# Performance work log

Hardware: AMD Instinct MI355X
Metric: run time of the kernel (lower is better)

## Reference

```python
import jax, jax.numpy as jnp
import numpy as np

# TISA RBF basis (helpers l2_dist / rbf_basis in the repo): f_i(d) = a_i * exp(-|b_i| * (d - c_i)^2)

def setup_inputs() -> dict:
    key = jax.random.key(0)
    k = jax.random.split(key, 8)
    B, L, H, D, S, F = 2, 2048, 8, 64, 2, 5
    qs = jax.random.normal(k[0], (B, L, H, D), dtype=jnp.float32)
    ks = jax.random.normal(k[1], (B, L, H, D), dtype=jnp.float32)
    vs = jax.random.normal(k[2], (B, L, H, D), dtype=jnp.float32)
    qs_s = jax.random.uniform(k[3], (B, L, S), dtype=jnp.float32)
    ks_s = jax.random.uniform(k[4], (B, L, S), dtype=jnp.float32)
    a = jax.random.uniform(k[5], (H * F,), dtype=jnp.float32)
    b = jax.random.uniform(k[6], (H * F,), dtype=jnp.float32)
    c = jax.random.normal(k[7], (H * F,), dtype=jnp.float32) * 0.5
    return {"qs": qs, "ks": ks, "vs": vs, "qs_s": qs_s, "ks_s": ks_s, "a": a, "b": b, "c": c}


def _tisa_attention(qs, ks, vs, qs_s, ks_s, a, b, c):
    B, Q, H, D = qs.shape
    F = a.size // H
    aH, bH, cH = (p.reshape(H, F) for p in (a, b, c))
    # pairwise euclidean distance between query and key locations: [B, Q, K]
    diff = qs_s[:, :, None, :] - ks_s[:, None, :, :]
    d = jnp.sqrt(jnp.sum(diff * diff, axis=-1))
    d_ = d[:, None]  # [B, 1, Q, K] broadcast over heads
    # RBF bias summed over F basis functions (small fixed F -> python sum avoids B,H,F,Q,K blowup)
    bias = sum(
        aH[:, f][None, :, None, None]
        * jnp.exp(-jnp.abs(bH[:, f])[None, :, None, None] * (d_ - cH[:, f][None, :, None, None]) ** 2)
        for f in range(F)
    )  # [B, H, Q, K]
    scale = 1.0 / jnp.sqrt(jnp.asarray(D, dtype=qs.dtype))
    scores = jnp.einsum('bqhd,bkhd->bhqk', qs * scale, ks) + bias
    attn = jax.nn.softmax(scores, axis=-1)
    return jnp.einsum('bhqk,bkhd->bqhd', attn, vs)


def reference(qs, ks, vs, qs_s, ks_s, a, b, c):
    # Matches scan_tisa_biased_attention: online-softmax chunking is mathematically
    # identical to a single stable softmax over the full key axis.
    return _tisa_attention(qs, ks, vs, qs_s, ks_s, a, b, c)
```

## Files before the change

kernel.cpp:

```cpp
#include <hip/hip_runtime.h>
#include <cmath>

typedef _Float16 half8 __attribute__((ext_vector_type(8)));
typedef _Float16 half2v __attribute__((ext_vector_type(2)));
typedef float f32x4 __attribute__((ext_vector_type(4)));
typedef float f32x2 __attribute__((ext_vector_type(2)));

#define B_ 2
#define L_ 2048
#define H_ 8
#define D_ 64
#define S_ 2
#define F_ 5
#define LUTN 512
#define LSCALE 362.03867f
#define LOG2E 1.44269504f
#define QSC (0.125f * LOG2E)

#define QOFF 0
#define KOFF 2097152
#define VOFF 4194304
#define WS_NEED 12582912

#define OFF_K 0
#define OFF_V 16384
#define OFF_P 32768
#define OFF_LUT 53248
#define OFF_KSS 57360
#define ARENA_SZ 59408
#define SLOTF (16 * 68 + 16)

#define GLOBAL_LOAD_LDS16(g, l)                                                  \
  __builtin_amdgcn_global_load_lds((const __attribute__((address_space(1))) void*)(g), \
                                   (__attribute__((address_space(3))) void*)(l), 16, 0, 0)

__global__ __launch_bounds__(256, 4)
void tisa_preproc(const float* __restrict__ qs, const float* __restrict__ ks,
                  const float* __restrict__ vs, _Float16* __restrict__ wsh) {
  __shared__ _Float16 Vl[64 * 72];
  const int t = threadIdx.x;
  const int u = blockIdx.x & 31;
  const int bh = blockIdx.x >> 5;
  const size_t base = ((size_t)(bh >> 3) * L_ + (size_t)u * 64) * (H_ * D_) + (size_t)(bh & 7) * D_;

#pragma unroll
  for (int jj = 0; jj < 2; ++jj) {
    int id = t * 2 + jj;
    int row = id >> 3, c = id & 7;
    const float* src = qs + base + (size_t)row * 512 + c * 8;
    f32x4 x0 = ((const f32x4*)src)[0], x1 = ((const f32x4*)src)[1];
    half8 hh;
#pragma unroll
    for (int k = 0; k < 4; ++k) { hh[k] = (_Float16)(x0[k] * QSC); hh[k + 4] = (_Float16)(x1[k] * QSC); }
    *(half8*)&wsh[QOFF + ((size_t)bh * 32 + u) * 4096 + row * 64 + (c ^ (row & 7)) * 8] = hh;
  }
#pragma unroll
  for (int jj = 0; jj < 2; ++jj) {
    int id = t * 2 + jj;
    int tile = id >> 8, row = (id >> 3) & 31, c = id & 7;
    const float* src = ks + base + (size_t)(tile * 32 + row) * 512 + c * 8;
    f32x4 x0 = ((const f32x4*)src)[0], x1 = ((const f32x4*)src)[1];
    half8 hh;
#pragma unroll
    for (int k = 0; k < 4; ++k) { hh[k] = (_Float16)x0[k]; hh[k + 4] = (_Float16)x1[k]; }
    *(half8*)&wsh[KOFF + ((size_t)bh * 64 + u * 2 + tile) * 2048 + row * 64 + (c ^ (row & 7)) * 8] = hh;
  }
  {
    int key = t >> 2, d0 = (t & 3) * 16;
    const float* src = vs + base + (size_t)key * 512 + d0;
    f32x4 a0 = ((const f32x4*)src)[0], a1 = ((const f32x4*)src)[1];
    f32x4 a2 = ((const f32x4*)src)[2], a3 = ((const f32x4*)src)[3];
    half8 h0, h1;
#pragma unroll
    for (int k = 0; k < 4; ++k) {
      h0[k] = (_Float16)a0[k]; h0[k + 4] = (_Float16)a1[k];
      h1[k] = (_Float16)a2[k]; h1[k + 4] = (_Float16)a3[k];
    }
    *(half8*)&Vl[key * 72 + d0] = h0;
    *(half8*)&Vl[key * 72 + d0 + 8] = h1;
  }
  __syncthreads();
#pragma unroll
  for (int jj = 0; jj < 2; ++jj) {
    int id = t * 2 + jj;
    int tile = id >> 8, s = (id >> 3) & 31, cp = id & 7;
    int d = 2 * s + (cp >> 2), kb = (cp & 3) * 8;
    half8 hh;
#pragma unroll
    for (int j = 0; j < 8; ++j) hh[j] = Vl[(tile * 32 + kb + j) * 72 + d];
    *(half8*)&wsh[VOFF + ((size_t)bh * 64 + u * 2 + tile) * 2048 + s * 64 + (cp ^ (s & 7)) * 8] = hh;
  }
}

__global__ __launch_bounds__(1024, 8)
void tisa_attn_main(const float* __restrict__ qs_s, const float* __restrict__ ks_s,
                    const float* __restrict__ ap, const float* __restrict__ bp,
                    const float* __restrict__ cp, const _Float16* __restrict__ wsh,
                    float* __restrict__ out) {
  __shared__ __align__(16) char arena[ARENA_SZ];
  f32x2* LUT2 = (f32x2*)(arena + OFF_LUT);

  const int t = threadIdx.x;
  const int lane = t & 63;
  const int w = t >> 6;
  const int g = w >> 2;
  const int qw = w & 3;
  const int t2 = t & 255;
  const int quad = lane >> 4;
  const int l16 = lane & 15;

  const int qt = blockIdx.x & 31;
  const int bh = blockIdx.x >> 5;
  const int h = bh & 7;
  const int b = bh >> 3;
  const int q0 = qt * 64;

  if (t <= LUTN) {
    float af[F_], nb[F_], cf[F_];
#pragma unroll
    for (int f = 0; f < F_; ++f) {
      af[f] = ap[h * F_ + f];
      nb[f] = -fabsf(bp[h * F_ + f]);
      cf[f] = cp[h * F_ + f];
    }
    float d0 = (float)t * (1.0f / LSCALE), d1 = (float)(t + 1) * (1.0f / LSCALE);
    float s0 = 0.f, s1 = 0.f;
#pragma unroll
    for (int f = 0; f < F_; ++f) {
      float e0 = d0 - cf[f], e1 = d1 - cf[f];
      s0 += af[f] * __expf(nb[f] * (e0 * e0));
      s1 += af[f] * __expf(nb[f] * (e1 * e1));
    }
    float v0 = (s0 - 8.0f) * LOG2E, v1 = (s1 - 8.0f) * LOG2E;
    LUT2[t] = (f32x2){v0, v1 - v0};
  }

  float qx[4], qy[4];
#pragma unroll
  for (int r = 0; r < 4; ++r) {
    int qrow = q0 + qw * 16 + quad * 4 + r;
    qx[r] = qs_s[((size_t)b * L_ + qrow) * 2 + 0] * LSCALE;
    qy[r] = qs_s[((size_t)b * L_ + qrow) * 2 + 1] * LSCALE;
  }

  const _Float16* Qt = wsh + QOFF + ((size_t)bh * 32 + qt) * 4096;
  const _Float16* Kbh = wsh + KOFF + (size_t)bh * 64 * 2048;
  const _Float16* Vbh = wsh + VOFF + (size_t)bh * 64 * 2048;

  if (w < 8)
    GLOBAL_LOAD_LDS16(Qt + w * 512 + lane * 8, arena + OFF_K + w * 1024);
  __syncthreads();

  half8 qA[2];
#pragma unroll
  for (int kb = 0; kb < 2; ++kb)
    qA[kb] = *(const half8*)(arena + OFF_K + (qw * 16 + l16) * 128 +
                             ((kb * 4 + quad) ^ (l16 & 7)) * 16);

  f32x4 oc[4];
#pragma unroll
  for (int df = 0; df < 4; ++df) oc[df] = (f32x4){0.f, 0.f, 0.f, 0.f};
  float lsum[4] = {0.f, 0.f, 0.f, 0.f};

  const _Float16* ksrc = Kbh + (size_t)(g * 16) * 2048 + t2 * 8;
  const _Float16* vsrc = Vbh + (size_t)(g * 16) * 2048 + t2 * 8;
  char* kdst = arena + OFF_K + g * 4096 + qw * 1024;
  char* vdst = arena + OFF_V + g * 4096 + qw * 1024;
  f32x2* kssG = (f32x2*)(arena + OFF_KSS + g * 512);
  _Float16* Pw = (_Float16*)(arena + OFF_P + w * 1280 + quad * 320 + l16 * 2);

  for (int it = 0; it < 16; ++it) {
    __syncthreads();
    GLOBAL_LOAD_LDS16(ksrc, kdst);
    GLOBAL_LOAD_LDS16(vsrc, vdst);
    ksrc += 2048; vsrc += 2048;
    if (t2 < 32) {
      f32x2 c = *(const f32x2*)(ks_s + ((size_t)b * L_ + (g * 16 + it) * 32 + t2) * 2);
      kssG[t2] = (f32x2){c.x * LSCALE, c.y * LSCALE};
    }
    __syncthreads();

    f32x4 acc[2];
#pragma unroll
    for (int nf = 0; nf < 2; ++nf) {
      f32x4 a = (f32x4){0.f, 0.f, 0.f, 0.f};
#pragma unroll
      for (int kb = 0; kb < 2; ++kb) {
        half8 kf = *(const half8*)(arena + OFF_K + g * 4096 + (nf * 16 + l16) * 128 +
                                   ((kb * 4 + quad) ^ (l16 & 7)) * 16);
        a = __builtin_amdgcn_mfma_f32_16x16x32_f16(qA[kb], kf, a, 0, 0, 0);
      }
      acc[nf] = a;
    }

#pragma unroll
    for (int nf = 0; nf < 2; ++nf) {
      f32x2 kc = kssG[nf * 16 + l16];
#pragma unroll
      for (int r = 0; r < 4; ++r) {
        float dx = qx[r] - kc.x, dy = qy[r] - kc.y;
        float tt = sqrtf(fmaf(dx, dx, dy * dy));
        int ii = (int)tt;
        float fr = tt - (float)ii;
        f32x2 e = LUT2[ii];
        float p = __builtin_amdgcn_exp2f(acc[nf][r] + fmaf(fr, e.y, e.x));
        acc[nf][r] = p;
        lsum[r] += p;
        Pw[r * 40 + nf * 16] = (_Float16)p;
      }
    }

    half8 pa = *(const half8*)(arena + OFF_P + w * 1280 + l16 * 80 + quad * 16);
#pragma unroll
    for (int df = 0; df < 4; ++df) {
      half8 vf = *(const half8*)(arena + OFF_V + g * 4096 + (l16 >> 1) * 128 + df * 1024 +
                                 ((((l16 & 1) * 4 + quad) ^ ((l16 >> 1) & 7)) * 16));
      oc[df] = __builtin_amdgcn_mfma_f32_16x16x32_f16(pa, vf, oc[df], 0, 0, 0);
    }
  }

  float lred[4];
#pragma unroll
  for (int r = 0; r < 4; ++r) {
    float s = lsum[r];
    s += __shfl_xor(s, 1);
    s += __shfl_xor(s, 2);
    s += __shfl_xor(s, 4);
    s += __shfl_xor(s, 8);
    lred[r] = s;
  }
  __syncthreads();
  float* slots = (float*)arena;
  if (g >= 2) {
    float* sl = slots + ((g - 2) * 4 + qw) * SLOTF;
#pragma unroll
    for (int df = 0; df < 4; ++df)
#pragma unroll
      for (int r = 0; r < 4; ++r)
        sl[(quad * 4 + r) * 68 + df * 16 + l16] = oc[df][r];
    if (l16 == 0) {
#pragma unroll
      for (int r = 0; r < 4; ++r) sl[16 * 68 + quad * 4 + r] = lred[r];
    }
  }
  __syncthreads();
  if (g < 2) {
    float* sl = slots + (g * 4 + qw) * SLOTF;
#pragma unroll
    for (int df = 0; df < 4; ++df)
#pragma unroll
      for (int r = 0; r < 4; ++r)
        oc[df][r] += sl[(quad * 4 + r) * 68 + df * 16 + l16];
#pragma unroll
    for (int r = 0; r < 4; ++r) lred[r] += sl[16 * 68 + quad * 4 + r];
  }
  if (g == 1) {
    float* sl = slots + (4 + qw) * SLOTF;
#pragma unroll
    for (int df = 0; df < 4; ++df)
#pragma unroll
      for (int r = 0; r < 4; ++r)
        sl[(quad * 4 + r) * 68 + df * 16 + l16] = oc[df][r];
    if (l16 == 0) {
#pragma unroll
      for (int r = 0; r < 4; ++r) sl[16 * 68 + quad * 4 + r] = lred[r];
    }
  }
  __syncthreads();
  if (g == 0) {
    float* sl = slots + (4 + qw) * SLOTF;
    float inv_l[4];
#pragma unroll
    for (int r = 0; r < 4; ++r)
      inv_l[r] = 1.f / (lred[r] + sl[16 * 68 + quad * 4 + r]);
#pragma unroll
    for (int df = 0; df < 4; ++df)
#pragma unroll
      for (int r = 0; r < 4; ++r) {
        int qrow = q0 + qw * 16 + quad * 4 + r;
        float v = oc[df][r] + sl[(quad * 4 + r) * 68 + df * 16 + l16];
        out[((size_t)(b * L_ + qrow)) * (H_ * D_) + h * D_ + df * 16 + l16] = v * inv_l[r];
      }
  }
}

#define KSTR 72
#define PH 72
__global__ __launch_bounds__(512, 4)
void tisa_attn_fallback(const float* __restrict__ qs, const float* __restrict__ ks,
                        const float* __restrict__ vs, const float* __restrict__ qs_s,
                        const float* __restrict__ ks_s, const float* __restrict__ ap,
                        const float* __restrict__ bp, const float* __restrict__ cp,
                        float* __restrict__ out) {
  __shared__ _Float16 Ks[2][64 * KSTR];
  __shared__ _Float16 VT[2][D_ * KSTR];
  __shared__ _Float16 Pf[8][16 * PH];
  __shared__ float kss2[2][64 * 2];
  __shared__ f32x2 LUT2s[LUTN + 1];
  __shared__ float comb[4][16][64];
  __shared__ float combl[4][16];

  const int t = threadIdx.x;
  const int lane = t & 63;
  const int w = t >> 6;
  const int g = w >> 2;
  const int qw = w & 3;
  const int t2 = t & 255;
  const int quad = lane >> 4;
  const int l16 = lane & 15;
  const int qt = blockIdx.x & 31;
  const int bh = blockIdx.x >> 5;
  const int h = bh & 7;
  const int b = bh >> 3;
  const int q0 = qt * 64;

  float af[F_], nb[F_], cf[F_];
#pragma unroll
  for (int f = 0; f < F_; ++f) {
    af[f] = ap[h * F_ + f];
    nb[f] = -fabsf(bp[h * F_ + f]);
    cf[f] = cp[h * F_ + f];
  }
  for (int i = t; i <= LUTN; i += 512) {
    float d0 = (float)i * (1.0f / LSCALE), d1 = (float)(i + 1) * (1.0f / LSCALE);
    float s0 = 0.f, s1 = 0.f;
#pragma unroll
    for (int f = 0; f < F_; ++f) {
      float e0 = d0 - cf[f], e1 = d1 - cf[f];
      s0 += af[f] * __expf(nb[f] * (e0 * e0));
      s1 += af[f] * __expf(nb[f] * (e1 * e1));
    }
    LUT2s[i] = (f32x2){s0 - 8.0f, s1 - 8.0f};
  }
  float qx[4], qy[4];
#pragma unroll
  for (int r = 0; r < 4; ++r) {
    int qrow = q0 + qw * 16 + quad * 4 + r;
    qx[r] = qs_s[(b * L_ + qrow) * S_ + 0];
    qy[r] = qs_s[(b * L_ + qrow) * S_ + 1];
  }
  if (t < 256) {
    const int row = t >> 2, dc = (t & 3) * 16;
    const float* src = qs + (((size_t)(b * L_ + q0 + row)) * H_ + h) * D_ + dc;
    const f32x4* s4 = (const f32x4*)src;
    f32x4 v0 = s4[0], v1 = s4[1], v2 = s4[2], v3 = s4[3];
    half8 w0, w1;
#pragma unroll
    for (int u = 0; u < 4; ++u) {
      w0[u] = (_Float16)(v0[u] * 0.125f); w0[u + 4] = (_Float16)(v1[u] * 0.125f);
      w1[u] = (_Float16)(v2[u] * 0.125f); w1[u + 4] = (_Float16)(v3[u] * 0.125f);
    }
    *(half8*)&Ks[0][row * KSTR + dc] = w0;
    *(half8*)&Ks[0][row * KSTR + dc + 8] = w1;
  }
  __syncthreads();
  half8 qA[2];
#pragma unroll
  for (int kb = 0; kb < 2; ++kb)
    qA[kb] = *(const half8*)&Ks[0][(qw * 16 + l16) * KSTR + kb * 32 + quad * 8];
  f32x4 oc[4];
#pragma unroll
  for (int df = 0; df < 4; ++df) oc[df] = (f32x4){0.f, 0.f, 0.f, 0.f};
  float l_r[4] = {0.f, 0.f, 0.f, 0.f};

  for (int it = 0; it < 16; ++it) {
    const int k0 = (g * 16 + it) * 64;
    __syncthreads();
    {
      const int row = t2 >> 2, dc = (t2 & 3) * 16;
      const float* src = ks + (((size_t)(b * L_ + k0 + row)) * H_ + h) * D_ + dc;
      const f32x4* s4 = (const f32x4*)src;
      f32x4 v0 = s4[0], v1 = s4[1], v2 = s4[2], v3 = s4[3];
      half8 w0, w1;
#pragma unroll
      for (int u = 0; u < 4; ++u) {
        w0[u] = (_Float16)v0[u]; w0[u + 4] = (_Float16)v1[u];
        w1[u] = (_Float16)v2[u]; w1[u + 4] = (_Float16)v3[u];
      }
      *(half8*)&Ks[g][row * KSTR + dc] = w0;
      *(half8*)&Ks[g][row * KSTR + dc + 8] = w1;
    }
    {
      const int kk = (t2 & 31) * 2, dg = (t2 >> 5) * 8;
      const float* s0 = vs + (((size_t)(b * L_ + k0 + kk)) * H_ + h) * D_ + dg;
      const float* s1 = s0 + H_ * D_;
      f32x4 a0 = ((const f32x4*)s0)[0], a1 = ((const f32x4*)s0)[1];
      f32x4 b0 = ((const f32x4*)s1)[0], b1 = ((const f32x4*)s1)[1];
#pragma unroll
      for (int u = 0; u < 4; ++u) {
        half2v p0 = {(_Float16)a0[u], (_Float16)b0[u]};
        *(half2v*)&VT[g][(dg + u) * KSTR + kk] = p0;
        half2v p1 = {(_Float16)a1[u], (_Float16)b1[u]};
        *(half2v*)&VT[g][(dg + 4 + u) * KSTR + kk] = p1;
      }
    }
    if (t2 < 128) kss2[g][t2] = ks_s[((size_t)(b * L_) + k0 + (t2 >> 1)) * S_ + (t2 & 1)];
    __syncthreads();
    f32x4 acc[4];
#pragma unroll
    for (int nf = 0; nf < 4; ++nf) {
      f32x4 a = (f32x4){0.f, 0.f, 0.f, 0.f};
#pragma unroll
      for (int kb = 0; kb < 2; ++kb) {
        half8 kf = *(const half8*)&Ks[g][(nf * 16 + l16) * KSTR + kb * 32 + quad * 8];
        a = __builtin_amdgcn_mfma_f32_16x16x32_f16(qA[kb], kf, a, 0, 0, 0);
      }
      acc[nf] = a;
    }
#pragma unroll
    for (int nf = 0; nf < 4; ++nf) {
      float kx = kss2[g][(nf * 16 + l16) * 2 + 0];
      float ky = kss2[g][(nf * 16 + l16) * 2 + 1];
#pragma unroll
      for (int r = 0; r < 4; ++r) {
        float dx = qx[r] - kx, dy = qy[r] - ky;
        float dist = sqrtf(fmaf(dx, dx, dy * dy));
        float tt = dist * LSCALE;
        int ii = (int)tt;
        float fr = tt - (float)ii;
        f32x2 lh = LUT2s[ii];
        float p = __expf(acc[nf][r] + fmaf(fr, lh.y - lh.x, lh.x));
        acc[nf][r] = p;
      }
    }
#pragma unroll
    for (int r = 0; r < 4; ++r)
      l_r[r] += (acc[0][r] + acc[1][r]) + (acc[2][r] + acc[3][r]);
#pragma unroll
    for (int nf = 0; nf < 4; ++nf)
#pragma unroll
      for (int r = 0; r < 4; ++r)
        Pf[w][(quad * 4 + r) * PH + nf * 16 + l16] = (_Float16)acc[nf][r];
#pragma unroll
    for (int kb = 0; kb < 2; ++kb) {
      half8 pa = *(const half8*)&Pf[w][l16 * PH + kb * 32 + quad * 8];
#pragma unroll
      for (int df = 0; df < 4; ++df) {
        half8 vf = *(const half8*)&VT[g][(df * 16 + l16) * KSTR + kb * 32 + quad * 8];
        oc[df] = __builtin_amdgcn_mfma_f32_16x16x32_f16(pa, vf, oc[df], 0, 0, 0);
      }
    }
  }
  __syncthreads();
  float lred[4];
#pragma unroll
  for (int r = 0; r < 4; ++r) {
    float s = l_r[r];
    s += __shfl_xor(s, 1); s += __shfl_xor(s, 2);
    s += __shfl_xor(s, 4); s += __shfl_xor(s, 8);
    lred[r] = s;
  }
  if (g == 1) {
#pragma unroll
    for (int df = 0; df < 4; ++df)
#pragma unroll
      for (int r = 0; r < 4; ++r)
        comb[qw][quad * 4 + r][df * 16 + l16] = oc[df][r];
    if (l16 == 0) {
#pragma unroll
      for (int r = 0; r < 4; ++r) combl[qw][quad * 4 + r] = lred[r];
    }
  }
  __syncthreads();
  if (g == 0) {
    float inv_l[4];
#pragma unroll
    for (int r = 0; r < 4; ++r)
      inv_l[r] = 1.f / (lred[r] + combl[qw][quad * 4 + r]);
#pragma unroll
    for (int df = 0; df < 4; ++df)
#pragma unroll
      for (int r = 0; r < 4; ++r) {
        int qrow = q0 + qw * 16 + quad * 4 + r;
        float v = oc[df][r] + comb[qw][quad * 4 + r][df * 16 + l16];
        out[(((size_t)(b * L_ + qrow)) * H_ + h) * D_ + df * 16 + l16] = v * inv_l[r];
      }
  }
}

extern "C" void kernel_launch(void* const* d_in, const int* in_sizes, int n_in,
                              void* d_out, int out_size, void* d_ws, size_t ws_size,
                              hipStream_t stream) {
  const float* qs = (const float*)d_in[0];
  const float* ks = (const float*)d_in[1];
  const float* vs = (const float*)d_in[2];
  const float* qs_s = (const float*)d_in[3];
  const float* ks_s = (const float*)d_in[4];
  const float* ap = (const float*)d_in[5];
  const float* bp = (const float*)d_in[6];
  const float* cp = (const float*)d_in[7];
  float* out = (float*)d_out;

  if (ws_size >= (size_t)WS_NEED) {
    _Float16* wsh = (_Float16*)d_ws;
    tisa_preproc<<<dim3(512), dim3(256), 0, stream>>>(qs, ks, vs, wsh);
    tisa_attn_main<<<dim3(512), dim3(1024), 0, stream>>>(qs_s, ks_s, ap, bp, cp, wsh, out);
  } else {
    tisa_attn_fallback<<<dim3(512), dim3(512), 0, stream>>>(qs, ks, vs, qs_s, ks_s, ap, bp, cp, out);
  }
}
```

Baseline: 152.2 us.

## Use nearest-bin RBF LUT, MFMA row sums, and prescaled key positions

```diff
diff --git a/kernel.cpp b/kernel.cpp
--- a/kernel.cpp
+++ b/kernel.cpp
@@ -12,22 +12,23 @@
 #define D_ 64
 #define S_ 2
 #define F_ 5
-#define LUTN 512
-#define LSCALE 362.03867f
+#define LUTN 2048
+#define LSCALE 1448.1547f
 #define LOG2E 1.44269504f
 #define QSC (0.125f * LOG2E)
 
 #define QOFF 0
 #define KOFF 2097152
 #define VOFF 4194304
-#define WS_NEED 12582912
+#define SOFFH 6291456
+#define WS_NEED 12615680
 
 #define OFF_K 0
 #define OFF_V 16384
 #define OFF_P 32768
 #define OFF_LUT 53248
-#define OFF_KSS 57360
-#define ARENA_SZ 59408
+#define OFF_KSS 61456
+#define ARENA_SZ 62480
 #define SLOTF (16 * 68 + 16)
 
 #define GLOBAL_LOAD_LDS16(g, l)                                                  \
@@ -36,7 +37,8 @@
 
 __global__ __launch_bounds__(256, 4)
 void tisa_preproc(const float* __restrict__ qs, const float* __restrict__ ks,
-                  const float* __restrict__ vs, _Float16* __restrict__ wsh) {
+                  const float* __restrict__ vs, const float* __restrict__ ks_s,
+                  _Float16* __restrict__ wsh) {
   __shared__ _Float16 Vl[64 * 72];
   const int t = threadIdx.x;
   const int u = blockIdx.x & 31;
@@ -65,6 +67,14 @@
     for (int k = 0; k < 4; ++k) { hh[k] = (_Float16)x0[k]; hh[k + 4] = (_Float16)x1[k]; }
     *(half8*)&wsh[KOFF + ((size_t)bh * 64 + u * 2 + tile) * 2048 + row * 64 + (c ^ (row & 7)) * 8] = hh;
   }
+  if ((bh & 7) == 0 && t < 32) {
+    const int b = bh >> 3;
+    const float* src = ks_s + ((size_t)b * L_ + u * 64) * 2 + t * 4;
+    float* dst = (float*)(wsh + SOFFH) + ((size_t)b * L_ + u * 64) * 2 + t * 4;
+    f32x4 x = *(const f32x4*)src;
+    x *= LSCALE;
+    *(f32x4*)dst = x;
+  }
   {
     int key = t >> 2, d0 = (t & 3) * 16;
     const float* src = vs + base + (size_t)key * 512 + d0;
@@ -93,12 +103,11 @@
 }
 
 __global__ __launch_bounds__(1024, 8)
-void tisa_attn_main(const float* __restrict__ qs_s, const float* __restrict__ ks_s,
-                    const float* __restrict__ ap, const float* __restrict__ bp,
-                    const float* __restrict__ cp, const _Float16* __restrict__ wsh,
-                    float* __restrict__ out) {
+void tisa_attn_main(const float* __restrict__ qs_s, const float* __restrict__ ap,
+                    const float* __restrict__ bp, const float* __restrict__ cp,
+                    const _Float16* __restrict__ wsh, float* __restrict__ out) {
   __shared__ __align__(16) char arena[ARENA_SZ];
-  f32x2* LUT2 = (f32x2*)(arena + OFF_LUT);
+  float* LUT = (float*)(arena + OFF_LUT);
 
   const int t = threadIdx.x;
   const int lane = t & 63;
@@ -115,7 +124,7 @@
   const int b = bh >> 3;
   const int q0 = qt * 64;
 
-  if (t <= LUTN) {
+  {
     float af[F_], nb[F_], cf[F_];
 #pragma unroll
     for (int f = 0; f < F_; ++f) {
@@ -123,16 +132,16 @@
       nb[f] = -fabsf(bp[h * F_ + f]);
       cf[f] = cp[h * F_ + f];
     }
-    float d0 = (float)t * (1.0f / LSCALE), d1 = (float)(t + 1) * (1.0f / LSCALE);
-    float s0 = 0.f, s1 = 0.f;
-#pragma unroll
-    for (int f = 0; f < F_; ++f) {
-      float e0 = d0 - cf[f], e1 = d1 - cf[f];
-      s0 += af[f] * __expf(nb[f] * (e0 * e0));
-      s1 += af[f] * __expf(nb[f] * (e1 * e1));
-    }
-    float v0 = (s0 - 8.0f) * LOG2E, v1 = (s1 - 8.0f) * LOG2E;
-    LUT2[t] = (f32x2){v0, v1 - v0};
+    for (int i = t; i <= LUTN; i += 1024) {
+      float d = ((float)i + 0.5f) * (1.0f / LSCALE);
+      float s = 0.f;
+#pragma unroll
+      for (int f = 0; f < F_; ++f) {
+        float e = d - cf[f];
+        s += af[f] * __expf(nb[f] * (e * e));
+      }
+      LUT[i] = (s - 8.0f) * LOG2E;
+    }
   }
 
   float qx[4], qy[4];
@@ -146,6 +155,7 @@
   const _Float16* Qt = wsh + QOFF + ((size_t)bh * 32 + qt) * 4096;
   const _Float16* Kbh = wsh + KOFF + (size_t)bh * 64 * 2048;
   const _Float16* Vbh = wsh + VOFF + (size_t)bh * 64 * 2048;
+  const float* wsS = (const float*)(wsh + SOFFH);
 
   if (w < 8)
     GLOBAL_LOAD_LDS16(Qt + w * 512 + lane * 8, arena + OFF_K + w * 1024);
@@ -160,13 +170,17 @@
   f32x4 oc[4];
 #pragma unroll
   for (int df = 0; df < 4; ++df) oc[df] = (f32x4){0.f, 0.f, 0.f, 0.f};
-  float lsum[4] = {0.f, 0.f, 0.f, 0.f};
+  f32x4 lsacc = (f32x4){0.f, 0.f, 0.f, 0.f};
+  half8 onesv;
+#pragma unroll
+  for (int j = 0; j < 8; ++j) onesv[j] = (_Float16)1.0f;
 
   const _Float16* ksrc = Kbh + (size_t)(g * 16) * 2048 + t2 * 8;
   const _Float16* vsrc = Vbh + (size_t)(g * 16) * 2048 + t2 * 8;
+  const f32x2* ssrc = (const f32x2*)(wsS + ((size_t)b * L_ + g * 512) * 2);
   char* kdst = arena + OFF_K + g * 4096 + qw * 1024;
   char* vdst = arena + OFF_V + g * 4096 + qw * 1024;
-  f32x2* kssG = (f32x2*)(arena + OFF_KSS + g * 512);
+  f32x2* kssG = (f32x2*)(arena + OFF_KSS + g * 256);
   _Float16* Pw = (_Float16*)(arena + OFF_P + w * 1280 + quad * 320 + l16 * 2);
 
   for (int it = 0; it < 16; ++it) {
@@ -174,10 +188,8 @@
     GLOBAL_LOAD_LDS16(ksrc, kdst);
     GLOBAL_LOAD_LDS16(vsrc, vdst);
     ksrc += 2048; vsrc += 2048;
-    if (t2 < 32) {
-      f32x2 c = *(const f32x2*)(ks_s + ((size_t)b * L_ + (g * 16 + it) * 32 + t2) * 2);
-      kssG[t2] = (f32x2){c.x * LSCALE, c.y * LSCALE};
-    }
+    if (t2 < 32) kssG[t2] = ssrc[t2];
+    ssrc += 32;
     __syncthreads();
 
     f32x4 acc[2];
@@ -201,16 +213,14 @@
         float dx = qx[r] - kc.x, dy = qy[r] - kc.y;
         float tt = sqrtf(fmaf(dx, dx, dy * dy));
         int ii = (int)tt;
-        float fr = tt - (float)ii;
-        f32x2 e = LUT2[ii];
-        float p = __builtin_amdgcn_exp2f(acc[nf][r] + fmaf(fr, e.y, e.x));
+        float p = __builtin_amdgcn_exp2f(acc[nf][r] + LUT[ii]);
         acc[nf][r] = p;
-        lsum[r] += p;
         Pw[r * 40 + nf * 16] = (_Float16)p;
       }
     }
 
     half8 pa = *(const half8*)(arena + OFF_P + w * 1280 + l16 * 80 + quad * 16);
+    lsacc = __builtin_amdgcn_mfma_f32_16x16x32_f16(pa, onesv, lsacc, 0, 0, 0);
 #pragma unroll
     for (int df = 0; df < 4; ++df) {
       half8 vf = *(const half8*)(arena + OFF_V + g * 4096 + (l16 >> 1) * 128 + df * 1024 +
@@ -221,14 +231,7 @@
 
   float lred[4];
 #pragma unroll
-  for (int r = 0; r < 4; ++r) {
-    float s = lsum[r];
-    s += __shfl_xor(s, 1);
-    s += __shfl_xor(s, 2);
-    s += __shfl_xor(s, 4);
-    s += __shfl_xor(s, 8);
-    lred[r] = s;
-  }
+  for (int r = 0; r < 4; ++r) lred[r] = lsacc[r];
   __syncthreads();
   float* slots = (float*)arena;
   if (g >= 2) {
@@ -286,6 +289,8 @@
 
 #define KSTR 72
 #define PH 72
+#define FLUTN 512
+#define FLSCALE 362.03867f
 __global__ __launch_bounds__(512, 4)
 void tisa_attn_fallback(const float* __restrict__ qs, const float* __restrict__ ks,
                         const float* __restrict__ vs, const float* __restrict__ qs_s,
@@ -296,7 +301,7 @@
   __shared__ _Float16 VT[2][D_ * KSTR];
   __shared__ _Float16 Pf[8][16 * PH];
   __shared__ float kss2[2][64 * 2];
-  __shared__ f32x2 LUT2s[LUTN + 1];
+  __shared__ f32x2 LUT2s[FLUTN + 1];
   __shared__ float comb[4][16][64];
   __shared__ float combl[4][16];
 
@@ -321,8 +326,8 @@
     nb[f] = -fabsf(bp[h * F_ + f]);
     cf[f] = cp[h * F_ + f];
   }
-  for (int i = t; i <= LUTN; i += 512) {
-    float d0 = (float)i * (1.0f / LSCALE), d1 = (float)(i + 1) * (1.0f / LSCALE);
+  for (int i = t; i <= FLUTN; i += 512) {
+    float d0 = (float)i * (1.0f / FLSCALE), d1 = (float)(i + 1) * (1.0f / FLSCALE);
     float s0 = 0.f, s1 = 0.f;
 #pragma unroll
     for (int f = 0; f < F_; ++f) {
@@ -415,7 +420,7 @@
       for (int r = 0; r < 4; ++r) {
         float dx = qx[r] - kx, dy = qy[r] - ky;
         float dist = sqrtf(fmaf(dx, dx, dy * dy));
-        float tt = dist * LSCALE;
+        float tt = dist * FLSCALE;
         int ii = (int)tt;
         float fr = tt - (float)ii;
         f32x2 lh = LUT2s[ii];
@@ -493,8 +498,8 @@
 
   if (ws_size >= (size_t)WS_NEED) {
     _Float16* wsh = (_Float16*)d_ws;
-    tisa_preproc<<<dim3(512), dim3(256), 0, stream>>>(qs, ks, vs, wsh);
-    tisa_attn_main<<<dim3(512), dim3(1024), 0, stream>>>(qs_s, ks_s, ap, bp, cp, wsh, out);
+    tisa_preproc<<<dim3(512), dim3(256), 0, stream>>>(qs, ks, vs, ks_s, wsh);
+    tisa_attn_main<<<dim3(512), dim3(1024), 0, stream>>>(qs_s, ap, bp, cp, wsh, out);
   } else {
     tisa_attn_fallback<<<dim3(512), dim3(512), 0, stream>>>(qs, ks, vs, qs_s, ks_s, ap, bp, cp, out);
   }
```

New measurement: 150.8 us. About the same (-0.9%).
